# Optimization experiments

Measured on AMD Instinct MI355X. Metric: run time of the kernel, lower is better.

Reference implementation:

```python
import jax, jax.numpy as jnp
import numpy as np

N = 50000      # nodes
E = 800000     # edges (avg degree 16)
C = 16         # hidden states per generative model
M = 32         # discrete symbol alphabet size
G = 8          # n_gen


def setup_inputs() -> dict:
    key = jax.random.key(0)
    k = jax.random.split(key, 6)
    u = lambda kk, shp: jax.random.uniform(kk, shp, jnp.float32, -5.0, 5.0)
    return {
        "x": jax.random.randint(k[0], (N,), 0, M),
        "edge_index": jax.random.randint(k[1], (2, E), 0, N),
        "B0": u(k[2], (C, M, G)),       # CGMMLayer_0.B
        "Pi": u(k[3], (C, G)),          # CGMMLayer_0.Pi
        "B1": u(k[4], (C, M, G)),       # CGMMLayer.B
        "Q_neigh": u(k[5], (C, C, G)),  # CGMMLayer.Q_neigh
    }


def reference(x, edge_index, B0, Pi, B1, Q_neigh):
    n = x.shape[0]
    # ---- layer 0 (CGMMLayer_0) ----
    sm_B0 = jax.nn.softmax(B0, axis=1)   # [C,M,G], softmax over symbols
    sm_Pi = jax.nn.softmax(Pi, axis=0)   # [C,G],   softmax over states
    # unnorm_posterior = Pi * B[:, x]    -> [N,C,G]
    unnorm0 = sm_Pi[None, :, :] * jnp.transpose(sm_B0[:, x, :], (1, 0, 2))
    norm0 = unnorm0.sum(1, keepdims=True)           # [N,1,G]
    ll0 = jnp.log(norm0[:, 0, :])                   # [N,G]
    post0 = unnorm0 / norm0                         # [N,C,G] = h_prev
    # ---- layer 1 (CGMMLayer) ----
    sm_Q = jax.nn.softmax(Q_neigh, axis=0)          # [C,C,G], softmax over dim 0
    sm_B1 = jax.nn.softmax(B1, axis=1)              # [C,M,G]
    src, dst = edge_index[0], edge_index[1]
    gathered = post0[dst]                           # [E,C,G] edge gather
    aggr_sum = jax.ops.segment_sum(gathered, src, num_segments=n)   # [N,C,G]
    cnt = jax.ops.segment_sum(jnp.ones((src.shape[0],), jnp.float32), src, num_segments=n)
    aggr = aggr_sum / jnp.maximum(cnt, 1.0)[:, None, None]          # scatter-mean
    B_nodes = jnp.transpose(sm_B1[:, x, :], (1, 0, 2))[:, :, None, :]  # [N,C,1,G]
    # joint over (current state i, neighbor state l): [N,C,C,G]
    unnorm1 = B_nodes * sm_Q[None, :, :, :] * aggr[:, None, :, :]
    norm1 = unnorm1.sum((1, 2), keepdims=True)      # [N,1,1,G]
    post1 = (unnorm1 / norm1).sum(2)                # [N,C,G] posterior_i
    ll1 = jnp.log(norm1[:, 0, 0, :])                # [N,G]
    log_likelihood = jnp.stack([ll0, ll1], axis=1)  # [N,2,G] (per layer)
    return log_likelihood, post1
```

## Files before the change

### kernel.cpp

```cpp
#include <hip/hip_runtime.h>
#include <hip/hip_bf16.h>
#include <math.h>

#define Nn 50000
#define Ee 800000
#define Cc 16
#define Mm 32
#define Gg 8
#define CAP 64

#define P1B 256
#define NBK 512
#define BSZ 98
#define SEGCAP 24
#define L0B 510

__device__ __forceinline__ float ldin(const void* p, int idx, int isbf) {
    if (isbf) return __bfloat162float(((const __hip_bfloat16*)p)[idx]);
    return ((const float*)p)[idx];
}
__device__ __forceinline__ void stout(void* p, size_t idx, float v, int isbf) {
    if (isbf) ((__hip_bfloat16*)p)[idx] = __float2bfloat16(v);
    else ((float*)p)[idx] = v;
}
__device__ __forceinline__ unsigned short f2bf(float f) {
    unsigned u = __float_as_uint(f);
    return (unsigned short)((u + 0x7FFFu + ((u >> 16) & 1u)) >> 16);
}
__device__ __forceinline__ float bflo(unsigned v) { return __uint_as_float(v << 16); }
__device__ __forceinline__ float bfhi(unsigned v) { return __uint_as_float(v & 0xffff0000u); }

__device__ __forceinline__ int detect_bf16(const void* B0, int tid, int* sflag) {
    if (tid < 64) {
        unsigned wv = ((const unsigned*)B0)[tid];
        unsigned ex = (wv >> 7) & 0xFFu;
        unsigned long long m = __ballot(ex >= 120u && ex <= 130u);
        if (tid == 0) *sflag = (__popcll(m) >= 48) ? 1 : 0;
    }
    __syncthreads();
    return *sflag;
}

__device__ __forceinline__ void sm_col(float* a, int base, int stride, int cnt) {
    float mx = -1e30f;
    for (int k = 0; k < cnt; ++k) mx = fmaxf(mx, a[base + k * stride]);
    float s = 0.f;
    for (int k = 0; k < cnt; ++k) {
        float e = __expf(a[base + k * stride] - mx);
        a[base + k * stride] = e;
        s += e;
    }
    float inv = 1.0f / s;
    for (int k = 0; k < cnt; ++k) a[base + k * stride] *= inv;
}

__global__ void bucket_layer0(const int* __restrict__ ei,
                              const int* __restrict__ x,
                              const void* __restrict__ B0,
                              const void* __restrict__ Pi,
                              const void* __restrict__ B1,
                              const void* __restrict__ Q,
                              unsigned* __restrict__ segbuf,
                              int* __restrict__ segcnt,
                              unsigned short* __restrict__ post0,
                              float* __restrict__ smB1ws,
                              float* __restrict__ smQgws,
                              int* __restrict__ flag_ws,
                              void* __restrict__ out) {
    int b = blockIdx.x, tid = threadIdx.x;
    __shared__ unsigned shb[NBK + NBK * SEGCAP];
    __shared__ int sflag;

    if (b < P1B) {
        int* scnt = (int*)shb;
        unsigned* sstage = shb + NBK;
        for (int i = tid; i < NBK; i += 256) scnt[i] = 0;
        __syncthreads();
        const int base = b * (Ee / P1B);
        const int end  = base + (Ee / P1B);
        for (int e = base + tid; e < end; e += 256) {
            int s = ei[e];
            int d = ei[Ee + e];
            int bk = s / BSZ;
            int pos = atomicAdd(&scnt[bk], 1);
            if (pos < SEGCAP)
                sstage[bk * SEGCAP + pos] = ((unsigned)(s - bk * BSZ) << 16) | (unsigned)d;
        }
        __syncthreads();
        unsigned* myseg = segbuf + (size_t)b * (NBK * SEGCAP);
        for (int idx = tid; idx < NBK * SEGCAP; idx += 256) {
            int bk = idx / SEGCAP;
            int i  = idx - bk * SEGCAP;
            int c  = scnt[bk]; c = c < SEGCAP ? c : SEGCAP;
            if (i < c) myseg[idx] = sstage[idx];
        }
        for (int i = tid; i < NBK; i += 256) {
            int c = scnt[i]; c = c < SEGCAP ? c : SEGCAP;
            segcnt[b * NBK + i] = c;
        }
        return;
    }

    float* sh = (float*)shb;

    if (b == P1B + L0B) {
        if (tid < 16) {
            uint4 z; z.x = 0u; z.y = 0u; z.z = 0u; z.w = 0u;
            ((uint4*)(post0 + (size_t)Nn * 128))[tid] = z;
        }
        const int isbf = detect_bf16(B0, tid, &sflag);
        if (tid == 0) flag_ws[0] = isbf;
        for (int i = tid; i < Cc * Mm * Gg; i += 256) sh[i] = ldin(B1, i, isbf);
        __syncthreads();
        if (tid < 128) sm_col(sh, (tid >> 3) * (Mm * Gg) + (tid & 7), Gg, Mm);
        __syncthreads();
        for (int i = tid; i < Cc * Mm * Gg; i += 256) smB1ws[i] = sh[i];
        __syncthreads();
        for (int i = tid; i < Cc * Cc * Gg; i += 256) sh[i] = ldin(Q, i, isbf);
        __syncthreads();
        if (tid < 128) sm_col(sh, (tid >> 3) * Gg + (tid & 7), Cc * Gg, Cc);
        __syncthreads();
        for (int t = tid; t < Cc * Cc * Gg; t += 256) {
            int i = t >> 7, rem = t & 127, l = rem >> 3, g = rem & 7;
            smQgws[g * (Cc * Cc) + i * Cc + l] = sh[t];
        }
        return;
    }

    float* sB0sm = sh;
    float* sPism = sh + 4096;
    const int isbf = detect_bf16(B0, tid, &sflag);

    for (int i = tid; i < Cc * Mm * Gg; i += 256) sB0sm[i] = ldin(B0, i, isbf);
    if (tid < Cc * Gg) sPism[tid] = ldin(Pi, tid, isbf);
    __syncthreads();
    if (tid < 128) {
        sm_col(sB0sm, (tid >> 3) * (Mm * Gg) + (tid & 7), Gg, Mm);
    } else if (tid < 128 + Gg) {
        sm_col(sPism, tid - 128, Gg, Cc);
    }
    __syncthreads();

    for (int idx = (b - P1B) * 256 + tid; idx < Nn * Gg; idx += L0B * 256) {
        int n = idx >> 3, g = idx & 7;
        int xv = x[n];
        float u[Cc];
        float norm = 0.f;
#pragma unroll
        for (int c = 0; c < Cc; ++c) {
            float v = sPism[c * Gg + g] * sB0sm[c * (Mm * Gg) + xv * Gg + g];
            u[c] = v; norm += v;
        }
        float inv = 1.0f / norm;
        unsigned short h[Cc];
#pragma unroll
        for (int c = 0; c < Cc; ++c) h[c] = f2bf(u[c] * inv);
        uint4 w0, w1;
        w0.x = h[0] | (h[1] << 16);   w0.y = h[2] | (h[3] << 16);
        w0.z = h[4] | (h[5] << 16);   w0.w = h[6] | (h[7] << 16);
        w1.x = h[8] | (h[9] << 16);   w1.y = h[10] | (h[11] << 16);
        w1.z = h[12] | (h[13] << 16); w1.w = h[14] | (h[15] << 16);
        uint4* dst = (uint4*)(post0 + (size_t)n * 128 + g * 16);
        dst[0] = w0; dst[1] = w1;
        stout(out, (size_t)n * (2 * Gg) + g, logf(norm), isbf);
    }
}

#define GL2(vv, eb, nn, dde) { int ej_ = (eb) + sub16; \
    int dn_ = (ej_ < (dde)) ? (int)list[(nn) * CAP + ej_] : Nn; \
    unsigned off_ = ((unsigned)dn_ << 8) + mbyte; \
    vv = *(const uint4*)((const char*)post0 + off_); }
#define GACC(vv) { \
    acc[0] += bflo(vv.x); acc[1] += bfhi(vv.x); acc[2] += bflo(vv.y); acc[3] += bfhi(vv.y); \
    acc[4] += bflo(vv.z); acc[5] += bfhi(vv.z); acc[6] += bflo(vv.w); acc[7] += bfhi(vv.w); }

__global__ __launch_bounds__(512) void place_aggr(
        const unsigned* __restrict__ segbuf,
        const int* __restrict__ segcnt,
        const unsigned short* __restrict__ post0,
        const int* __restrict__ x,
        const float* __restrict__ smB1ws,
        const float* __restrict__ smQgws,
        const int* __restrict__ flag_ws,
        void* __restrict__ out) {
    __shared__ unsigned list[BSZ * CAP];
    __shared__ int cnt[BSZ];
    __shared__ float sQ[4341];
    int b = blockIdx.x, tid = threadIdx.x;
    const int isbf = flag_ws[0];

    for (int t = tid; t < Cc * Cc * Gg; t += 512) {
        int g = t >> 8, i = (t >> 4) & 15, j = t & 15;
        sQ[g * 545 + i * 34 + j] = smQgws[t];
    }
    for (int i = tid; i < BSZ; i += 512) cnt[i] = 0;
    __syncthreads();

    {
        int seg = tid & 255, half = tid >> 8;
        int c = segcnt[seg * NBK + b];
        const unsigned* sp = segbuf + ((size_t)seg * NBK + b) * SEGCAP;
        for (int i = half; i < c; i += 2) {
            unsigned pk = sp[i];
            int sl = (int)(pk >> 16);
            int d  = (int)(pk & 0xffffu);
            int pos = atomicAdd(&cnt[sl], 1);
            if (pos < CAP) list[sl * CAP + pos] = (unsigned)d;
        }
    }
    __syncthreads();

    const int lane = tid & 63, wib = tid >> 6;
    const int sub16 = lane >> 4;
    const unsigned mbyte = (unsigned)((lane & 15) * 16);
    const int ii = lane >> 3, gW = lane & 7;
    const int i0 = 2 * ii, i1 = i0 + 1;
    const float* qp = sQ + gW * 545 + i0 * 34;
    const int nbase = b * BSZ;
    int limt = Nn - nbase; if (limt > BSZ) limt = BSZ;
    const int lim = limt;

    int n = wib;
    int dv0 = 0, dd0 = 0; float b0c = 0.f, b1c = 0.f;
    uint4 bA0, bA1, bA2, bA3;
    bA0.x = bA0.y = bA0.z = bA0.w = 0u; bA1 = bA0; bA2 = bA0; bA3 = bA0;
    if (n < lim) {
        dv0 = __builtin_amdgcn_readfirstlane(cnt[n]);
        dd0 = dv0 < CAP ? dv0 : CAP;
        int xv = x[nbase + n];
        b0c = smB1ws[i0 * (Mm * Gg) + xv * Gg + gW];
        b1c = smB1ws[i1 * (Mm * Gg) + xv * Gg + gW];
        GL2(bA0, 0, n, dd0); GL2(bA1, 4, n, dd0); GL2(bA2, 8, n, dd0); GL2(bA3, 12, n, dd0);
    }

    while (n < lim) {
        int n1 = n + 8;
        int dv1 = 0, dd1 = 0; float b0n = 0.f, b1n = 0.f;
        uint4 bB0, bB1, bB2, bB3;
        bB0.x = bB0.y = bB0.z = bB0.w = 0u; bB1 = bB0; bB2 = bB0; bB3 = bB0;
        if (n1 < lim) {
            dv1 = __builtin_amdgcn_readfirstlane(cnt[n1]);
            dd1 = dv1 < CAP ? dv1 : CAP;
            int xv = x[nbase + n1];
            b0n = smB1ws[i0 * (Mm * Gg) + xv * Gg + gW];
            b1n = smB1ws[i1 * (Mm * Gg) + xv * Gg + gW];
            GL2(bB0, 0, n1, dd1); GL2(bB1, 4, n1, dd1); GL2(bB2, 8, n1, dd1); GL2(bB3, 12, n1, dd1);
        }

        float acc[8];
#pragma unroll
        for (int j = 0; j < 8; ++j) acc[j] = 0.f;
        GACC(bA0); GACC(bA1); GACC(bA2); GACC(bA3);
        for (int e = 16; e < dd0; e += 16) {
            uint4 t0, t1, t2, t3;
            GL2(t0, e, n, dd0); GL2(t1, e + 4, n, dd0);
            GL2(t2, e + 8, n, dd0); GL2(t3, e + 12, n, dd0);
            GACC(t0); GACC(t1); GACC(t2); GACC(t3);
        }

#pragma unroll
        for (int j = 0; j < 8; ++j) {
            acc[j] += __shfl_xor(acc[j], 16, 64);
            acc[j] += __shfl_xor(acc[j], 32, 64);
        }
        float qa0 = 0.f, qa1 = 0.f;
#pragma unroll
        for (int j = 0; j < 8; ++j) {
            float t0 = __shfl(acc[j], 2 * gW, 64);
            float t1 = __shfl(acc[j], 2 * gW + 1, 64);
            qa0 += qp[j] * t0 + qp[8 + j] * t1;
            qa1 += qp[34 + j] * t0 + qp[42 + j] * t1;
        }
        float invd = 1.0f / fmaxf((float)dv0, 1.0f);
        qa0 *= invd; qa1 *= invd;
        float v0 = b0c * qa0, v1 = b1c * qa1;
        float nrm = v0 + v1;
        nrm += __shfl_xor(nrm, 8, 64);
        nrm += __shfl_xor(nrm, 16, 64);
        nrm += __shfl_xor(nrm, 32, 64);
        float invn = 1.0f / nrm;
        int ng = nbase + n;
        size_t pbase = (size_t)Nn * 2 * Gg + (size_t)ng * (Cc * Gg);
        stout(out, pbase + i0 * Gg + gW, v0 * invn, isbf);
        stout(out, pbase + i1 * Gg + gW, v1 * invn, isbf);
        if (ii == 0) stout(out, (size_t)ng * (2 * Gg) + Gg + gW, logf(nrm), isbf);

        n = n1;
        dv0 = dv1; dd0 = dd1; b0c = b0n; b1c = b1n;
        bA0 = bB0; bA1 = bB1; bA2 = bB2; bA3 = bB3;
    }
}

extern "C" void kernel_launch(void* const* d_in, const int* in_sizes, int n_in,
                              void* d_out, int out_size, void* d_ws, size_t ws_size,
                              hipStream_t stream) {
    const int* x  = (const int*)d_in[0];
    const int* ei = (const int*)d_in[1];
    const void* B0 = d_in[2];
    const void* Pi = d_in[3];
    const void* B1 = d_in[4];
    const void* Q  = d_in[5];

    float* ws = (float*)d_ws;
    int*   flag   = (int*)ws;
    float* smB1ws = ws + 128;
    float* smQgws = smB1ws + 4096;
    unsigned short* post0 = (unsigned short*)(smQgws + 2048);
    int* segcnt     = (int*)(post0 + (size_t)(Nn + 1) * 128);
    unsigned* segbuf = (unsigned*)(segcnt + P1B * NBK);

    bucket_layer0<<<P1B + L0B + 1, 256, 0, stream>>>(
        ei, x, B0, Pi, B1, Q, segbuf, segcnt, post0, smB1ws, smQgws, flag, d_out);

    place_aggr<<<NBK, 512, 0, stream>>>(
        segbuf, segcnt, post0, x, smB1ws, smQgws, flag, d_out);
}
```

Baseline: 132.7 us.

## Split aggregation buckets across two blocks and vectorize edge-index loads

The edge-bucketing phase now reads source and destination indices as int4 vectors over 250 blocks of 3200 edges each, instead of scalar loads over 256 blocks. The aggregation kernel launches twice as many blocks, each handling half of a 98-node bucket, so each block has 49 nodes of work and a smaller shared list. This is meant to raise parallelism and occupancy in the gather/aggregate phase. The cost is that every segment is read twice, once by each half-block, with entries outside the half filtered out. Layer-0 block count is bumped to compensate.

```diff
diff --git a/kernel.cpp b/kernel.cpp
--- a/kernel.cpp
+++ b/kernel.cpp
@@ -9,11 +9,12 @@
 #define Gg 8
 #define CAP 64
 
-#define P1B 256
+#define P1B 250
 #define NBK 512
 #define BSZ 98
+#define HBS 49
 #define SEGCAP 24
-#define L0B 510
+#define L0B 517
 
 __device__ __forceinline__ float ldin(const void* p, int idx, int isbf) {
     if (isbf) return __bfloat162float(((const __hip_bfloat16*)p)[idx]);
@@ -76,15 +77,20 @@
         unsigned* sstage = shb + NBK;
         for (int i = tid; i < NBK; i += 256) scnt[i] = 0;
         __syncthreads();
-        const int base = b * (Ee / P1B);
-        const int end  = base + (Ee / P1B);
-        for (int e = base + tid; e < end; e += 256) {
-            int s = ei[e];
-            int d = ei[Ee + e];
-            int bk = s / BSZ;
-            int pos = atomicAdd(&scnt[bk], 1);
-            if (pos < SEGCAP)
-                sstage[bk * SEGCAP + pos] = ((unsigned)(s - bk * BSZ) << 16) | (unsigned)d;
+        const int4* ei4 = (const int4*)ei;
+        const int qbase = b * 800;
+        for (int q = tid; q < 800; q += 256) {
+            int4 sv = ei4[qbase + q];
+            int4 dv = ei4[200000 + qbase + q];
+#pragma unroll
+            for (int k = 0; k < 4; ++k) {
+                int s = (k == 0) ? sv.x : (k == 1) ? sv.y : (k == 2) ? sv.z : sv.w;
+                int d = (k == 0) ? dv.x : (k == 1) ? dv.y : (k == 2) ? dv.z : dv.w;
+                int bk = s / BSZ;
+                int pos = atomicAdd(&scnt[bk], 1);
+                if (pos < SEGCAP)
+                    sstage[bk * SEGCAP + pos] = ((unsigned)(s - bk * BSZ) << 16) | (unsigned)d;
+            }
         }
         __syncthreads();
         unsigned* myseg = segbuf + (size_t)b * (NBK * SEGCAP);
@@ -183,29 +189,34 @@
         const float* __restrict__ smQgws,
         const int* __restrict__ flag_ws,
         void* __restrict__ out) {
-    __shared__ unsigned list[BSZ * CAP];
-    __shared__ int cnt[BSZ];
+    __shared__ unsigned list[HBS * CAP];
+    __shared__ int cnt[HBS];
     __shared__ float sQ[4341];
-    int b = blockIdx.x, tid = threadIdx.x;
+    int bb = blockIdx.x, tid = threadIdx.x;
+    const int b = bb >> 1, h49 = (bb & 1) * HBS;
     const int isbf = flag_ws[0];
 
     for (int t = tid; t < Cc * Cc * Gg; t += 512) {
         int g = t >> 8, i = (t >> 4) & 15, j = t & 15;
         sQ[g * 545 + i * 34 + j] = smQgws[t];
     }
-    for (int i = tid; i < BSZ; i += 512) cnt[i] = 0;
+    for (int i = tid; i < HBS; i += 512) cnt[i] = 0;
     __syncthreads();
 
     {
         int seg = tid & 255, half = tid >> 8;
-        int c = segcnt[seg * NBK + b];
-        const unsigned* sp = segbuf + ((size_t)seg * NBK + b) * SEGCAP;
-        for (int i = half; i < c; i += 2) {
-            unsigned pk = sp[i];
-            int sl = (int)(pk >> 16);
-            int d  = (int)(pk & 0xffffu);
-            int pos = atomicAdd(&cnt[sl], 1);
-            if (pos < CAP) list[sl * CAP + pos] = (unsigned)d;
+        if (seg < P1B) {
+            int c = segcnt[seg * NBK + b];
+            const unsigned* sp = segbuf + ((size_t)seg * NBK + b) * SEGCAP;
+            for (int i = half; i < c; i += 2) {
+                unsigned pk = sp[i];
+                int sl = (int)(pk >> 16) - h49;
+                if ((unsigned)sl < HBS) {
+                    int d = (int)(pk & 0xffffu);
+                    int pos = atomicAdd(&cnt[sl], 1);
+                    if (pos < CAP) list[sl * CAP + pos] = (unsigned)d;
+                }
+            }
         }
     }
     __syncthreads();
@@ -216,8 +227,8 @@
     const int ii = lane >> 3, gW = lane & 7;
     const int i0 = 2 * ii, i1 = i0 + 1;
     const float* qp = sQ + gW * 545 + i0 * 34;
-    const int nbase = b * BSZ;
-    int limt = Nn - nbase; if (limt > BSZ) limt = BSZ;
+    const int nbase = b * BSZ + h49;
+    int limt = Nn - nbase; if (limt > HBS) limt = HBS;
     const int lim = limt;
 
     int n = wib;
@@ -312,6 +323,6 @@
     bucket_layer0<<<P1B + L0B + 1, 256, 0, stream>>>(
         ei, x, B0, Pi, B1, Q, segbuf, segcnt, post0, smB1ws, smQgws, flag, d_out);
 
-    place_aggr<<<NBK, 512, 0, stream>>>(
+    place_aggr<<<2 * NBK, 512, 0, stream>>>(
         segbuf, segcnt, post0, x, smB1ws, smQgws, flag, d_out);
 }
```

Result: slower. 141.1 us (+6.3%).

## Transpose segment buffer layout and vectorize edge loads in bucketing pass

Applied to the files above, without the earlier changes.

The bucketing blocks now read edge indices as int4 vectors, and the split changes to 250 blocks so each handles exactly 3200 edges. The segment buffer and counts are stored bucket-major, so each place_aggr block reads one contiguous strip instead of gathering 256 strided segments. The consumer stages the counts in shared memory and scans the full strip with all 512 threads, skipping slots past each count. In exchange, the producer's writes become scattered and the consumer reads unused padding slots.

```diff
diff --git a/kernel.cpp b/kernel.cpp
--- a/kernel.cpp
+++ b/kernel.cpp
@@ -9,11 +9,11 @@
 #define Gg 8
 #define CAP 64
 
-#define P1B 256
+#define P1B 250
 #define NBK 512
 #define BSZ 98
 #define SEGCAP 24
-#define L0B 510
+#define L0B 517
 
 __device__ __forceinline__ float ldin(const void* p, int idx, int isbf) {
     if (isbf) return __bfloat162float(((const __hip_bfloat16*)p)[idx]);
@@ -76,27 +76,32 @@
         unsigned* sstage = shb + NBK;
         for (int i = tid; i < NBK; i += 256) scnt[i] = 0;
         __syncthreads();
-        const int base = b * (Ee / P1B);
-        const int end  = base + (Ee / P1B);
-        for (int e = base + tid; e < end; e += 256) {
-            int s = ei[e];
-            int d = ei[Ee + e];
-            int bk = s / BSZ;
-            int pos = atomicAdd(&scnt[bk], 1);
-            if (pos < SEGCAP)
-                sstage[bk * SEGCAP + pos] = ((unsigned)(s - bk * BSZ) << 16) | (unsigned)d;
-        }
-        __syncthreads();
-        unsigned* myseg = segbuf + (size_t)b * (NBK * SEGCAP);
+        const int4* ei4 = (const int4*)ei;
+        const int qbase = b * 800;
+        for (int q = tid; q < 800; q += 256) {
+            int4 sv = ei4[qbase + q];
+            int4 dv = ei4[200000 + qbase + q];
+#pragma unroll
+            for (int k = 0; k < 4; ++k) {
+                int s = (k == 0) ? sv.x : (k == 1) ? sv.y : (k == 2) ? sv.z : sv.w;
+                int d = (k == 0) ? dv.x : (k == 1) ? dv.y : (k == 2) ? dv.z : dv.w;
+                int bk = s / BSZ;
+                int pos = atomicAdd(&scnt[bk], 1);
+                if (pos < SEGCAP)
+                    sstage[bk * SEGCAP + pos] = ((unsigned)(s - bk * BSZ) << 16) | (unsigned)d;
+            }
+        }
+        __syncthreads();
         for (int idx = tid; idx < NBK * SEGCAP; idx += 256) {
             int bk = idx / SEGCAP;
             int i  = idx - bk * SEGCAP;
             int c  = scnt[bk]; c = c < SEGCAP ? c : SEGCAP;
-            if (i < c) myseg[idx] = sstage[idx];
+            if (i < c)
+                segbuf[((size_t)bk * P1B + b) * SEGCAP + i] = sstage[idx];
         }
         for (int i = tid; i < NBK; i += 256) {
             int c = scnt[i]; c = c < SEGCAP ? c : SEGCAP;
-            segcnt[b * NBK + i] = c;
+            segcnt[i * P1B + b] = c;
         }
         return;
     }
@@ -185,6 +190,7 @@
         void* __restrict__ out) {
     __shared__ unsigned list[BSZ * CAP];
     __shared__ int cnt[BSZ];
+    __shared__ int scl[P1B];
     __shared__ float sQ[4341];
     int b = blockIdx.x, tid = threadIdx.x;
     const int isbf = flag_ws[0];
@@ -194,18 +200,20 @@
         sQ[g * 545 + i * 34 + j] = smQgws[t];
     }
     for (int i = tid; i < BSZ; i += 512) cnt[i] = 0;
+    if (tid < P1B) scl[tid] = segcnt[b * P1B + tid];
     __syncthreads();
 
     {
-        int seg = tid & 255, half = tid >> 8;
-        int c = segcnt[seg * NBK + b];
-        const unsigned* sp = segbuf + ((size_t)seg * NBK + b) * SEGCAP;
-        for (int i = half; i < c; i += 2) {
-            unsigned pk = sp[i];
-            int sl = (int)(pk >> 16);
-            int d  = (int)(pk & 0xffffu);
-            int pos = atomicAdd(&cnt[sl], 1);
-            if (pos < CAP) list[sl * CAP + pos] = (unsigned)d;
+        const unsigned* strip = segbuf + (size_t)b * (P1B * SEGCAP);
+        for (int w = tid; w < P1B * SEGCAP; w += 512) {
+            unsigned pk = strip[w];
+            int seg = w / SEGCAP;
+            int i   = w - seg * SEGCAP;
+            if (i < scl[seg]) {
+                int sl = (int)(pk >> 16);
+                int pos = atomicAdd(&cnt[sl], 1);
+                if (pos < CAP) list[sl * CAP + pos] = pk & 0xffffu;
+            }
         }
     }
     __syncthreads();
@@ -307,7 +315,7 @@
     float* smQgws = smB1ws + 4096;
     unsigned short* post0 = (unsigned short*)(smQgws + 2048);
     int* segcnt     = (int*)(post0 + (size_t)(Nn + 1) * 128);
-    unsigned* segbuf = (unsigned*)(segcnt + P1B * NBK);
+    unsigned* segbuf = (unsigned*)(segcnt + NBK * P1B);
 
     bucket_layer0<<<P1B + L0B + 1, 256, 0, stream>>>(
         ei, x, B0, Pi, B1, Q, segbuf, segcnt, post0, smB1ws, smQgws, flag, d_out);
```

After: 132.2 us. About the same (-0.4%).
